# Kernel tuning notes

Hardware: AMD Instinct MI355X
Metric: run time of the kernel (lower is better)

## Reference

```python
import jax, jax.numpy as jnp
import numpy as np
import math

N = 4096      # n_history
D = 512       # embed_dim
H = 8         # time-weight MLP hidden size


def setup_inputs() -> dict:
    key = jax.random.key(0)
    k1, k2, k3, k4, k5 = jax.random.split(key, 5)
    return {
        "query_code_embeds": jax.random.normal(k1, (N, D), dtype=jnp.float32),
        "hist_embeddings": jax.random.normal(k2, (N, D), dtype=jnp.float32),
        "hist_times": jax.random.uniform(k3, (N,), dtype=jnp.float32),
        "tw_w1": jax.random.normal(k4, (1, H), dtype=jnp.float32) * (1.0 / math.sqrt(1.0)),
        "tw_b1": jnp.zeros((H,), dtype=jnp.float32),
        "tw_w2": jax.random.normal(k5, (H, 1), dtype=jnp.float32) * (1.0 / math.sqrt(H)),
        "tw_b2": jnp.zeros((1,), dtype=jnp.float32),
    }


def reference(query_code_embeds, hist_embeddings, hist_times, tw_w1, tw_b1, tw_w2, tw_b2):
    # pairwise absolute time differences: [n, n, 1]
    time_diffs = jnp.abs(hist_times[:, None] - hist_times[None, :])[..., None]
    # pointwise MLP on time diffs -> multiplicative attention bias [n, n]
    h = jax.nn.relu(time_diffs @ tw_w1 + tw_b1)            # [n, n, H]
    time_weights = jax.nn.sigmoid(h @ tw_w2 + tw_b2)[..., 0]  # [n, n]
    # scaled dot-product scores modulated by time weights
    scores = (query_code_embeds @ hist_embeddings.T) / math.sqrt(D)
    scores = scores * time_weights
    attn = jax.nn.softmax(scores, axis=1)
    return attn @ hist_embeddings
```

## Files before the change

### kernel.cpp

```cpp
#include <hip/hip_runtime.h>

#define N 4096
#define D 512
#define FRAG_SH 512
#define NTHR 256
#define NTHR_QK 512
#define SC_STRIDE 136
#define SMEM_BYTES 69632
#define BUF_SH 12288
#define PV_BUF_SH 18432
#define PV_SMEM_BYTES 73728

typedef __attribute__((ext_vector_type(8))) short short8;
typedef __attribute__((ext_vector_type(4))) float f32x4;
typedef const __attribute__((address_space(1))) unsigned int* gptr_t;
typedef __attribute__((address_space(3))) unsigned int* lptr_t;

__device__ __forceinline__ unsigned short f2bf(float f) {
    unsigned int u = __float_as_uint(f);
    u = (u + 0x7FFFu + ((u >> 16) & 1u)) >> 16;
    return (unsigned short)u;
}
__device__ __forceinline__ unsigned short f2bf_rn(float f) {
    return (unsigned short)((__float_as_uint(f) + 0x8000u) >> 16);
}
__device__ __forceinline__ float bf2f(unsigned short u) {
    return __uint_as_float((unsigned)u << 16);
}

__global__ __launch_bounds__(NTHR) void prep_kernel(
    const float* __restrict__ q, const float* __restrict__ hist,
    unsigned short* __restrict__ Qblk, unsigned short* __restrict__ Kblk,
    unsigned short* __restrict__ Vblk, float* __restrict__ dsum)
{
    __shared__ unsigned short smem[32 * 512];
    const int bid = blockIdx.x, tid = threadIdx.x;
    if (bid >= 256) {
        int z = (bid - 256) * NTHR + tid;
        #pragma unroll
        for (int j = 0; j < 8; ++j) dsum[z * 8 + j] = 0.f;
        return;
    }
    const bool isQ = bid < 128;
    const int t = isQ ? bid : bid - 128;
    const float* src = isQ ? q : hist;
    const float scale = isQ ? 0.04419417382415922f : 1.0f;

    #pragma unroll
    for (int k = 0; k < 16; ++k) {
        int idx = tid + k * 256;
        int row = idx >> 7;
        int c4  = (idx & 127) << 2;
        float4 v = *(const float4*)(src + (size_t)(t * 32 + row) * D + c4);
        ushort4 o;
        o.x = f2bf(v.x * scale); o.y = f2bf(v.y * scale);
        o.z = f2bf(v.z * scale); o.w = f2bf(v.w * scale);
        *(ushort4*)(smem + row * 512 + c4) = o;
    }
    __syncthreads();

    unsigned short* ABdst = isQ ? Qblk : Kblk;
    #pragma unroll
    for (int k = 0; k < 8; ++k) {
        int s = tid + k * 256;
        int fl = s >> 6, ln = s & 63;
        int dk = fl >> 1, rbl = fl & 1;
        int l16 = ln & 15, qq = ln >> 4;
        short8 v = *(const short8*)(smem + (rbl * 16 + l16) * 512 + dk * 32 + qq * 8);
        *(short8*)(ABdst + ((size_t)dk * 256 + t * 2 + rbl) * FRAG_SH + ln * 8) = v;
    }
    if (!isQ) {
        #pragma unroll
        for (int k = 0; k < 8; ++k) {
            int s = tid + k * 256;
            int db = s >> 6, ln = s & 63;
            int l16 = ln & 15, qq = ln >> 4;
            unsigned short tmp[8];
            #pragma unroll
            for (int j = 0; j < 8; ++j)
                tmp[j] = smem[(qq * 8 + j) * 512 + db * 16 + l16];
            *(short8*)(Vblk + ((size_t)t * 32 + db) * FRAG_SH + ln * 8) = *(const short8*)tmp;
        }
    }
}

__global__ __launch_bounds__(NTHR_QK, 4) void qk_kernel(
    const unsigned short* __restrict__ Qblk, const unsigned short* __restrict__ Kblk,
    const float* __restrict__ times,
    const float* __restrict__ w1, const float* __restrict__ b1,
    const float* __restrict__ w2, const float* __restrict__ b2,
    unsigned short* __restrict__ Pblk, float* __restrict__ dsum)
{
    extern __shared__ unsigned short smem[];
    const int tid = threadIdx.x, bid = blockIdx.x;
    const int wv = tid >> 6, lane = tid & 63;
    const int qq = lane >> 4, l16 = lane & 15;
    const int wy = wv >> 1, wx = wv & 1;
    const int cg = ((bid & 7) << 1) | ((bid >> 3) & 1);
    const int rg = bid >> 4;

    f32x4 acc[2][8];
    #pragma unroll
    for (int fy = 0; fy < 2; ++fy)
        #pragma unroll
        for (int fx = 0; fx < 8; ++fx) acc[fy][fx] = (f32x4){0.f, 0.f, 0.f, 0.f};

    auto stage = [&](int dk, int buf) {
        unsigned short* ldsb = smem + buf * BUF_SH;
        #pragma unroll
        for (int j = 0; j < 3; ++j) {
            const int s = wv * 3 + j;
            const unsigned short* g = (s < 8)
                ? (Qblk + ((size_t)dk * 256 + rg * 8 + s) * FRAG_SH + lane * 8)
                : (Kblk + ((size_t)dk * 256 + cg * 16 + (s - 8)) * FRAG_SH + lane * 8);
            __builtin_amdgcn_global_load_lds(
                (gptr_t)g, (lptr_t)(ldsb + s * FRAG_SH), 16, 0, 0);
        }
    };
    auto compute = [&](int buf) {
        const unsigned short* bufc = smem + buf * BUF_SH;
        short8 fa[2], fb[8];
        #pragma unroll
        for (int fy = 0; fy < 2; ++fy)
            fa[fy] = *(const short8*)(bufc + (wy * 2 + fy) * FRAG_SH + lane * 8);
        #pragma unroll
        for (int fx = 0; fx < 8; ++fx)
            fb[fx] = *(const short8*)(bufc + (8 + wx * 8 + fx) * FRAG_SH + lane * 8);
        #pragma unroll
        for (int fy = 0; fy < 2; ++fy)
            #pragma unroll
            for (int fx = 0; fx < 8; ++fx)
                acc[fy][fx] = __builtin_amdgcn_mfma_f32_16x16x32_bf16(fa[fy], fb[fx], acc[fy][fx], 0, 0, 0);
    };

    stage(0, 0);
    #pragma unroll 1
    for (int dk = 0; dk < 16; ++dk) {
        if (dk + 1 < 16) {
            stage(dk + 1, (dk + 1) & 1);
            asm volatile("s_waitcnt vmcnt(3)" ::: "memory");
        } else {
            asm volatile("s_waitcnt vmcnt(0)" ::: "memory");
        }
        __builtin_amdgcn_s_barrier();
        compute(dk & 1);
        __builtin_amdgcn_s_barrier();
    }

    float w1v[8], b1v[8], w2v[8];
    #pragma unroll
    for (int k = 0; k < 8; ++k) { w1v[k] = w1[k]; b1v[k] = b1[k]; w2v[k] = w2[k]; }
    const float b2v = b2[0];
    bool fast = true;
    #pragma unroll
    for (int k = 0; k < 8; ++k) fast = fast && (b1v[k] == 0.0f);
    float C1 = 0.0f;
    #pragma unroll
    for (int k = 0; k < 8; ++k) C1 += w2v[k] * fmaxf(w1v[k], 0.0f);

    const int rowbase = rg * 128 + wy * 32;
    const int colbase = cg * 256 + wx * 128;
    float tcol[8];
    #pragma unroll
    for (int fx = 0; fx < 8; ++fx) tcol[fx] = times[colbase + fx * 16 + l16];
    float trow[8];
    #pragma unroll
    for (int fy = 0; fy < 2; ++fy)
        #pragma unroll
        for (int ri = 0; ri < 4; ++ri)
            trow[fy * 4 + ri] = times[rowbase + fy * 16 + qq * 4 + ri];

    unsigned short* sc = smem + wv * (32 * SC_STRIDE);
    #pragma unroll
    for (int fy = 0; fy < 2; ++fy) {
        #pragma unroll
        for (int ri = 0; ri < 4; ++ri) {
            const float tq = trow[fy * 4 + ri];
            float se = 0.f;
            #pragma unroll
            for (int fx = 0; fx < 8; ++fx) {
                float td = fabsf(tq - tcol[fx]);
                float a = fmaf(td, C1, b2v);
                if (!fast) {
                    a = b2v;
                    #pragma unroll
                    for (int k = 0; k < 8; ++k)
                        a += w2v[k] * fmaxf(fmaf(td, w1v[k], b1v[k]), 0.f);
                }
                float twt = __builtin_amdgcn_rcpf(1.0f + __expf(-a));
                float e = __expf(acc[fy][fx][ri] * twt);
                se += e;
                sc[(fy * 16 + qq * 4 + ri) * SC_STRIDE + fx * 16 + l16] = f2bf_rn(e);
            }
            se += __shfl_xor(se, 1);
            se += __shfl_xor(se, 2);
            se += __shfl_xor(se, 4);
            se += __shfl_xor(se, 8);
            if (l16 == 0) atomicAdd(dsum + rowbase + fy * 16 + qq * 4 + ri, se);
        }
    }
    #pragma unroll
    for (int fy = 0; fy < 2; ++fy)
        #pragma unroll
        for (int kb2 = 0; kb2 < 4; ++kb2) {
            short8 v = *(const short8*)(sc + (fy * 16 + l16) * SC_STRIDE + kb2 * 32 + qq * 8);
            size_t fidx = (size_t)(cg * 8 + wx * 4 + kb2) * 256 + (rg * 8 + wy * 2 + fy);
            *(short8*)(Pblk + fidx * FRAG_SH + lane * 8) = v;
        }
}

__global__ __launch_bounds__(NTHR, 2) void pv_staged_kernel(
    const unsigned short* __restrict__ Pblk, const unsigned short* __restrict__ Vblk,
    unsigned short* __restrict__ Opart, int iters)
{
    extern __shared__ unsigned short smem[];
    const int tid = threadIdx.x;
    const int wv = tid >> 6, lane = tid & 63;
    const int qq = lane >> 4, l16 = lane & 15;
    const int chunk = blockIdx.x;
    const int rg = blockIdx.y;
    const int kbase = chunk * iters;

    f32x4 acc[4][8];
    #pragma unroll
    for (int fy = 0; fy < 4; ++fy)
        #pragma unroll
        for (int fx = 0; fx < 8; ++fx) acc[fy][fx] = (f32x4){0.f, 0.f, 0.f, 0.f};

    auto stage = [&](int it, int buf) {
        const int kb32 = kbase + it;
        unsigned short* ldsb = smem + buf * PV_BUF_SH;
        #pragma unroll
        for (int j = 0; j < 9; ++j) {
            const int s = wv * 9 + j;
            const unsigned short* g = (s < 4)
                ? (Pblk + ((size_t)kb32 * 256 + rg * 4 + s) * FRAG_SH + lane * 8)
                : (Vblk + ((size_t)kb32 * 32 + (s - 4)) * FRAG_SH + lane * 8);
            __builtin_amdgcn_global_load_lds(
                (gptr_t)g, (lptr_t)(ldsb + s * FRAG_SH), 16, 0, 0);
        }
    };
    auto compute = [&](int buf) {
        const unsigned short* bufc = smem + buf * PV_BUF_SH;
        short8 a[4], b[8];
        #pragma unroll
        for (int fy = 0; fy < 4; ++fy)
            a[fy] = *(const short8*)(bufc + fy * FRAG_SH + lane * 8);
        #pragma unroll
        for (int fx = 0; fx < 8; ++fx)
            b[fx] = *(const short8*)(bufc + (4 + wv * 8 + fx) * FRAG_SH + lane * 8);
        #pragma unroll
        for (int fy = 0; fy < 4; ++fy)
            #pragma unroll
            for (int fx = 0; fx < 8; ++fx)
                acc[fy][fx] = __builtin_amdgcn_mfma_f32_16x16x32_bf16(a[fy], b[fx], acc[fy][fx], 0, 0, 0);
    };

    stage(0, 0);
    #pragma unroll 1
    for (int it = 0; it < iters; ++it) {
        if (it + 1 < iters) {
            stage(it + 1, (it + 1) & 1);
            asm volatile("s_waitcnt vmcnt(9)" ::: "memory");
        } else {
            asm volatile("s_waitcnt vmcnt(0)" ::: "memory");
        }
        __builtin_amdgcn_s_barrier();
        compute(it & 1);
        __builtin_amdgcn_s_barrier();
    }

    unsigned short* ob = Opart + (size_t)chunk * N * D;
    #pragma unroll
    for (int fy = 0; fy < 4; ++fy)
        #pragma unroll
        for (int ri = 0; ri < 4; ++ri) {
            const int row = rg * 64 + fy * 16 + qq * 4 + ri;
            #pragma unroll
            for (int fx = 0; fx < 8; ++fx) {
                const int col = wv * 128 + fx * 16 + l16;
                ob[(size_t)row * D + col] = f2bf_rn(acc[fy][fx][ri]);
            }
        }
}

template<int FY>
__global__ __launch_bounds__(NTHR, 2) void pv_kernel(
    const unsigned short* __restrict__ Pblk, const unsigned short* __restrict__ Vblk,
    unsigned short* __restrict__ Opart, int iters)
{
    const int tid = threadIdx.x;
    const int wv = tid >> 6, lane = tid & 63;
    const int qq = lane >> 4, l16 = lane & 15;
    const int chunk = blockIdx.x;
    const int rg = blockIdx.y;
    const int kbase = chunk * iters;

    f32x4 acc[FY][8];
    #pragma unroll
    for (int fy = 0; fy < FY; ++fy)
        #pragma unroll
        for (int fx = 0; fx < 8; ++fx) acc[fy][fx] = (f32x4){0.f, 0.f, 0.f, 0.f};

    for (int it = 0; it < iters; ++it) {
        const int kb32 = kbase + it;
        short8 a[FY], b[8];
        #pragma unroll
        for (int fy = 0; fy < FY; ++fy)
            a[fy] = *(const short8*)(Pblk + ((size_t)kb32 * 256 + rg * FY + fy) * FRAG_SH + lane * 8);
        #pragma unroll
        for (int fx = 0; fx < 8; ++fx)
            b[fx] = *(const short8*)(Vblk + ((size_t)kb32 * 32 + wv * 8 + fx) * FRAG_SH + lane * 8);
        #pragma unroll
        for (int fy = 0; fy < FY; ++fy)
            #pragma unroll
            for (int fx = 0; fx < 8; ++fx)
                acc[fy][fx] = __builtin_amdgcn_mfma_f32_16x16x32_bf16(a[fy], b[fx], acc[fy][fx], 0, 0, 0);
    }

    unsigned short* ob = Opart + (size_t)chunk * N * D;
    #pragma unroll
    for (int fy = 0; fy < FY; ++fy)
        #pragma unroll
        for (int ri = 0; ri < 4; ++ri) {
            const int row = rg * (FY * 16) + fy * 16 + qq * 4 + ri;
            #pragma unroll
            for (int fx = 0; fx < 8; ++fx) {
                const int col = wv * 128 + fx * 16 + l16;
                ob[(size_t)row * D + col] = f2bf_rn(acc[fy][fx][ri]);
            }
        }
}

__global__ __launch_bounds__(NTHR) void reduce_kernel(
    const unsigned short* __restrict__ Opart, const float* __restrict__ dsum,
    float* __restrict__ out, int KS2)
{
    int i = blockIdx.x * NTHR + threadIdx.x;
    int row = i >> 6;
    float inv = 1.0f / dsum[row];
    float acc[8] = {0.f, 0.f, 0.f, 0.f, 0.f, 0.f, 0.f, 0.f};
    for (int c = 0; c < KS2; ++c) {
        short8 u = ((const short8*)(Opart + (size_t)c * N * D))[i];
        #pragma unroll
        for (int j = 0; j < 8; ++j) acc[j] += bf2f((unsigned short)u[j]);
    }
    float4 o0 = {acc[0] * inv, acc[1] * inv, acc[2] * inv, acc[3] * inv};
    float4 o1 = {acc[4] * inv, acc[5] * inv, acc[6] * inv, acc[7] * inv};
    ((float4*)out)[i * 2 + 0] = o0;
    ((float4*)out)[i * 2 + 1] = o1;
}

extern "C" void kernel_launch(void* const* d_in, const int* in_sizes, int n_in,
                              void* d_out, int out_size, void* d_ws, size_t ws_size,
                              hipStream_t stream) {
    const float* q     = (const float*)d_in[0];
    const float* hist  = (const float*)d_in[1];
    const float* times = (const float*)d_in[2];
    const float* w1    = (const float*)d_in[3];
    const float* b1    = (const float*)d_in[4];
    const float* w2    = (const float*)d_in[5];
    const float* b2    = (const float*)d_in[6];
    float* out = (float*)d_out;

    char* base = (char*)d_ws;
    const size_t MB4 = (size_t)N * D * 2;
    unsigned short* Vblk = (unsigned short*)base;
    unsigned short* Pblk = (unsigned short*)(base + MB4);
    float* dsum          = (float*)(base + MB4 + (size_t)N * (size_t)N * 2);
    char* ob             = base + MB4 + (size_t)N * (size_t)N * 2 + 65536;
    unsigned short* Qblk = (unsigned short*)ob;
    unsigned short* Kblk = (unsigned short*)(ob + MB4);
    unsigned short* Opart = (unsigned short*)ob;
    const size_t fixed = (size_t)(ob - base);
    const int KS2 = (ws_size >= fixed + 8 * MB4) ? 8 :
                    (ws_size >= fixed + 4 * MB4) ? 4 : 2;
    const int iters = (N / 32) / KS2;

    (void)hipFuncSetAttribute((const void*)qk_kernel,
                        hipFuncAttributeMaxDynamicSharedMemorySize, SMEM_BYTES);
    (void)hipFuncSetAttribute((const void*)pv_staged_kernel,
                        hipFuncAttributeMaxDynamicSharedMemorySize, PV_SMEM_BYTES);

    prep_kernel<<<258, NTHR, 0, stream>>>(q, hist, Qblk, Kblk, Vblk, dsum);
    qk_kernel<<<512, NTHR_QK, SMEM_BYTES, stream>>>(Qblk, Kblk, times, w1, b1, w2, b2, Pblk, dsum);
    if (KS2 == 8) {
        pv_staged_kernel<<<dim3(KS2, N / 64), NTHR, PV_SMEM_BYTES, stream>>>(Pblk, Vblk, Opart, iters);
    } else {
        pv_kernel<2><<<dim3(KS2, N / 32), NTHR, 0, stream>>>(Pblk, Vblk, Opart, iters);
    }
    reduce_kernel<<<(N * D / 8) / NTHR, NTHR, 0, stream>>>(Opart, dsum, out, KS2);
}
```

Measured before the change: 133.2 us.

## Load QK fragments directly from global memory instead of LDS double buffer

The QK score loop no longer stages Q and K fragments into a double-buffered LDS region with barriers. Each wave now reads its fragments straight from global memory into registers. The MFMA block is wrapped in s_setprio so compute-heavy waves get scheduling priority. This is meant to remove barrier and LDS round-trip overhead, at the cost of no software prefetch and redundant global reads across waves that previously shared staged tiles.

```diff
diff --git a/kernel.cpp b/kernel.cpp
--- a/kernel.cpp
+++ b/kernel.cpp
@@ -7,7 +7,6 @@
 #define NTHR_QK 512
 #define SC_STRIDE 136
 #define SMEM_BYTES 69632
-#define BUF_SH 12288
 #define PV_BUF_SH 18432
 #define PV_SMEM_BYTES 73728
 
@@ -105,46 +104,26 @@
         #pragma unroll
         for (int fx = 0; fx < 8; ++fx) acc[fy][fx] = (f32x4){0.f, 0.f, 0.f, 0.f};
 
-    auto stage = [&](int dk, int buf) {
-        unsigned short* ldsb = smem + buf * BUF_SH;
-        #pragma unroll
-        for (int j = 0; j < 3; ++j) {
-            const int s = wv * 3 + j;
-            const unsigned short* g = (s < 8)
-                ? (Qblk + ((size_t)dk * 256 + rg * 8 + s) * FRAG_SH + lane * 8)
-                : (Kblk + ((size_t)dk * 256 + cg * 16 + (s - 8)) * FRAG_SH + lane * 8);
-            __builtin_amdgcn_global_load_lds(
-                (gptr_t)g, (lptr_t)(ldsb + s * FRAG_SH), 16, 0, 0);
-        }
-    };
-    auto compute = [&](int buf) {
-        const unsigned short* bufc = smem + buf * BUF_SH;
+    const size_t DKSTEP = (size_t)256 * FRAG_SH;
+    const unsigned short* qptr = Qblk + (size_t)(rg * 8 + wy * 2) * FRAG_SH + lane * 8;
+    const unsigned short* kptr = Kblk + (size_t)(cg * 16 + wx * 8) * FRAG_SH + lane * 8;
+
+    #pragma unroll 1
+    for (int dk = 0; dk < 16; ++dk) {
+        const unsigned short* qb = qptr + (size_t)dk * DKSTEP;
+        const unsigned short* kb = kptr + (size_t)dk * DKSTEP;
         short8 fa[2], fb[8];
         #pragma unroll
-        for (int fy = 0; fy < 2; ++fy)
-            fa[fy] = *(const short8*)(bufc + (wy * 2 + fy) * FRAG_SH + lane * 8);
-        #pragma unroll
-        for (int fx = 0; fx < 8; ++fx)
-            fb[fx] = *(const short8*)(bufc + (8 + wx * 8 + fx) * FRAG_SH + lane * 8);
+        for (int fy = 0; fy < 2; ++fy) fa[fy] = *(const short8*)(qb + fy * FRAG_SH);
+        #pragma unroll
+        for (int fx = 0; fx < 8; ++fx) fb[fx] = *(const short8*)(kb + fx * FRAG_SH);
+        __builtin_amdgcn_s_setprio(1);
         #pragma unroll
         for (int fy = 0; fy < 2; ++fy)
             #pragma unroll
             for (int fx = 0; fx < 8; ++fx)
                 acc[fy][fx] = __builtin_amdgcn_mfma_f32_16x16x32_bf16(fa[fy], fb[fx], acc[fy][fx], 0, 0, 0);
-    };
-
-    stage(0, 0);
-    #pragma unroll 1
-    for (int dk = 0; dk < 16; ++dk) {
-        if (dk + 1 < 16) {
-            stage(dk + 1, (dk + 1) & 1);
-            asm volatile("s_waitcnt vmcnt(3)" ::: "memory");
-        } else {
-            asm volatile("s_waitcnt vmcnt(0)" ::: "memory");
-        }
-        __builtin_amdgcn_s_barrier();
-        compute(dk & 1);
-        __builtin_amdgcn_s_barrier();
+        __builtin_amdgcn_s_setprio(0);
     }
 
     float w1v[8], b1v[8], w2v[8];
```

New measurement: 139.3 us. +4.5%, slower.
